# Kernel optimization log

Measured on AMD Instinct MI355X. Metric: run time of the kernel, lower is better.

The kernel has to match this reference:

```python
import jax, jax.numpy as jnp
import numpy as np

EPS = 1e-08

def rms_norm(x, eps=EPS):
    # Matches torch: mean-centered, population variance (unbiased=False)
    mean = jnp.mean(x, axis=-1, keepdims=True)
    var = jnp.var(x, axis=-1, keepdims=True)
    return (x - mean) / jnp.sqrt(var + eps)

def activation_quant(x):
    s = 127.0 / jnp.max(jnp.abs(x), axis=-1, keepdims=True)
    return jnp.clip(jnp.round(s * x), -128, 127) / s

def ternary_matmul(x, w):
    # pos_mask - neg_mask of sign(w) equals sign(w); x @ sign(w).T
    return jnp.matmul(x, jnp.sign(w).T)

def setup_inputs() -> dict:
    key = jax.random.key(0)
    k0, k1, k2, k3 = jax.random.split(key, 4)
    B, S, D, H = 4, 2048, 2048, 8192
    x = jax.random.normal(k0, (B, S, D), dtype=jnp.float32)
    W_g = jax.random.normal(k1, (H, D), dtype=jnp.float32) * 0.01
    W_u = jax.random.normal(k2, (H, D), dtype=jnp.float32) * 0.01
    W_d = jax.random.normal(k3, (D, H), dtype=jnp.float32) * 0.01
    return {"x": x, "W_g": W_g, "W_u": W_u, "W_d": W_d}

def reference(x, W_g, W_u, W_d):
    xq = activation_quant(rms_norm(x))
    g = jax.nn.silu(ternary_matmul(xq, W_g))   # [B,S,H]
    u = ternary_matmul(xq, W_u)                # [B,S,H]
    p = g * u
    return ternary_matmul(p, W_d)              # [B,S,D]
```

## Files before the change

### kernel.cpp

```cpp
#include <hip/hip_runtime.h>
#include <stdint.h>

#define MROWS 8192
#define DDIM  2048
#define HDIM  8192

typedef __attribute__((ext_vector_type(8))) short bf16x8;
typedef __attribute__((ext_vector_type(4))) float f32x4;
typedef __attribute__((ext_vector_type(4))) int   i32x4;
typedef unsigned short u16;

__device__ __forceinline__ void async_load16(const void* g, void* l) {
  auto gp = reinterpret_cast<const __attribute__((address_space(1))) unsigned int*>(
      reinterpret_cast<uintptr_t>(g));
  auto lp = reinterpret_cast<__attribute__((address_space(3))) unsigned int*>(
      reinterpret_cast<uintptr_t>(l));
  __builtin_amdgcn_global_load_lds(gp, lp, 16, 0, 0);
}

__device__ __forceinline__ u16 f2bf(float f) {
  union { float f; unsigned int u; } v; v.f = f;
  unsigned int r = v.u + 0x7FFF + ((v.u >> 16) & 1);
  return (u16)(r >> 16);
}

__global__ void sign_i8x2_kernel(const float* __restrict__ wg, const float* __restrict__ wu,
                                 char* __restrict__ og, char* __restrict__ ou) {
  const int t = blockIdx.x * 256 + threadIdx.x;
  const float* w = blockIdx.y ? wu : wg;
  char* o = blockIdx.y ? ou : og;
  const float4* w4 = (const float4*)w;
  float4 a = w4[t * 2], b = w4[t * 2 + 1];
  float v[8] = {a.x, a.y, a.z, a.w, b.x, b.y, b.z, b.w};
  union { char s[8]; uint2 u; } pk;
#pragma unroll
  for (int i = 0; i < 8; i++)
    pk.s[i] = v[i] > 0.f ? (char)1 : (v[i] < 0.f ? (char)-1 : (char)0);
  ((uint2*)o)[t] = pk.u;
}

__global__ void sign_bf16_kernel(const float* __restrict__ w, u16* __restrict__ o) {
  const int t = blockIdx.x * 256 + threadIdx.x;
  const float4* w4 = (const float4*)w;
  float4 a = w4[t * 2], b = w4[t * 2 + 1];
  float v[8] = {a.x, a.y, a.z, a.w, b.x, b.y, b.z, b.w};
  union { u16 s[8]; uint4 u; } pk;
#pragma unroll
  for (int i = 0; i < 8; i++)
    pk.s[i] = v[i] > 0.f ? 0x3F80 : (v[i] < 0.f ? 0xBF80 : 0);
  ((uint4*)o)[t] = pk.u;
}

__global__ void norm_quant_i8_kernel(const float* __restrict__ x,
                                     char* __restrict__ q, float* __restrict__ inv) {
  const int row  = blockIdx.x;
  const int tid  = threadIdx.x;
  const int lane = tid & 63, wave = tid >> 6;
  const float4* xr = (const float4*)(x + (size_t)row * DDIM);
  float4 a = xr[tid * 2], b = xr[tid * 2 + 1];
  float v[8] = {a.x, a.y, a.z, a.w, b.x, b.y, b.z, b.w};
  float s1 = 0.f, s2 = 0.f;
#pragma unroll
  for (int i = 0; i < 8; i++) { s1 += v[i]; s2 += v[i] * v[i]; }
#pragma unroll
  for (int o = 1; o < 64; o <<= 1) { s1 += __shfl_xor(s1, o); s2 += __shfl_xor(s2, o); }
  __shared__ float ssum[4], ssq[4], smax[4];
  if (lane == 0) { ssum[wave] = s1; ssq[wave] = s2; }
  __syncthreads();
  s1 = ssum[0] + ssum[1] + ssum[2] + ssum[3];
  s2 = ssq[0] + ssq[1] + ssq[2] + ssq[3];
  const float mean = s1 * (1.f / DDIM);
  const float var  = s2 * (1.f / DDIM) - mean * mean;
  const float rstd = rsqrtf(var + 1e-8f);
  float mx = 0.f;
#pragma unroll
  for (int i = 0; i < 8; i++) { v[i] = (v[i] - mean) * rstd; mx = fmaxf(mx, fabsf(v[i])); }
#pragma unroll
  for (int o = 1; o < 64; o <<= 1) mx = fmaxf(mx, __shfl_xor(mx, o));
  if (lane == 0) smax[wave] = mx;
  __syncthreads();
  mx = fmaxf(fmaxf(smax[0], smax[1]), fmaxf(smax[2], smax[3]));
  const float s = 127.f / mx;
  if (tid == 0) inv[row] = mx * (1.f / 127.f);
  union { char s8[8]; uint2 u; } pk;
#pragma unroll
  for (int i = 0; i < 8; i++) {
    float qq = rintf(v[i] * s);
    qq = fminf(fmaxf(qq, -128.f), 127.f);
    pk.s8[i] = (char)(int)qq;
  }
  ((uint2*)(q + (size_t)row * DDIM))[tid] = pk.u;
}

__global__ __launch_bounds__(512, 2) void gemm_glu_i8_kernel(
    const char* __restrict__ A,
    const char* __restrict__ Bg,
    const char* __restrict__ Bu,
    const float* __restrict__ inv,
    u16* __restrict__ P)
{
  constexpr int K  = DDIM;
  constexpr int NT = K / 128;
  const int l   = blockIdx.x + gridDim.x * blockIdx.y;
  const int xcd = l & 7;
  const int s_  = l >> 3;
  const int n0 = (xcd * 8 + (s_ & 7)) * 128;
  const int m0 = (s_ >> 3) * 256;
  const int tid  = threadIdx.x;
  const int lane = tid & 63, wave = tid >> 6;
  const int wm = wave >> 1, wn = wave & 1;
  const int quad = lane >> 4, l16 = lane & 15;

  __shared__ __align__(16) char lds[131072];

  i32x4 accg[4][4], accu[4][4];
  const i32x4 zero = {0, 0, 0, 0};
#pragma unroll
  for (int i = 0; i < 4; i++)
#pragma unroll
    for (int j = 0; j < 4; j++) { accg[i][j] = zero; accu[i][j] = zero; }

  const int arow = wm * 64 + l16;
  const int brow = wn * 64 + l16;
  const int swz  = (l16 & 7) << 4;

  const int rr  = tid >> 3;
  const int cbs = ((tid & 7) << 4) ^ ((rr & 7) << 4);
  const char* aSrc = A  + (size_t)(m0 + rr) * K + cbs;
  const char* gSrc = Bg + (size_t)(n0 + rr) * K + cbs;
  const char* uSrc = Bu + (size_t)(n0 + rr) * K + cbs;

#define STG_A(is) async_load16(aSrc + (size_t)(is) * 64 * K + k0n, bufN + (is) * 8192 + wave * 1024)
#define STG_G(is) async_load16(gSrc + (size_t)(is) * 64 * K + k0n, bufN + 32768 + (is) * 8192 + wave * 1024)
#define STG_U(is) async_load16(uSrc + (size_t)(is) * 64 * K + k0n, bufN + 49152 + (is) * 8192 + wave * 1024)
#define STG_TILE() do { STG_A(0); STG_A(1); STG_A(2); STG_A(3); \
                        STG_G(0); STG_G(1); STG_U(0); STG_U(1); } while (0)

  {
    char* bufN = lds;           const int k0n = 0;
    STG_TILE();
  }
  {
    char* bufN = lds + 65536;   const int k0n = 128;
    STG_TILE();
  }
  asm volatile("s_waitcnt vmcnt(8)" ::: "memory");
  __builtin_amdgcn_s_barrier();

  for (int t = 0; t < NT; ++t) {
    const char* bufC = lds + (size_t)(t & 1) * 65536;
    i32x4 a[4];
#pragma unroll
    for (int ks = 0; ks < 2; ++ks) {
#pragma unroll
      for (int jh = 0; jh < 2; ++jh) {
        const int koff = (ks * 64 + quad * 16) ^ swz;
        if (jh == 0) {
#pragma unroll
          for (int i = 0; i < 4; ++i)
            a[i] = *(const i32x4*)(bufC + (size_t)(arow + i * 16) * 128 + koff);
        }
        i32x4 bg[2], bu[2];
#pragma unroll
        for (int jj = 0; jj < 2; ++jj) {
          const int j = jh * 2 + jj;
          bg[jj] = *(const i32x4*)(bufC + 32768 + (size_t)(brow + j * 16) * 128 + koff);
          bu[jj] = *(const i32x4*)(bufC + 49152 + (size_t)(brow + j * 16) * 128 + koff);
        }
        __builtin_amdgcn_s_barrier();
        __builtin_amdgcn_s_setprio(1);
#pragma unroll
        for (int i = 0; i < 4; ++i)
#pragma unroll
          for (int jj = 0; jj < 2; ++jj) {
            const int j = jh * 2 + jj;
            accg[i][j] = __builtin_amdgcn_mfma_i32_16x16x64_i8(a[i], bg[jj], accg[i][j], 0, 0, 0);
            accu[i][j] = __builtin_amdgcn_mfma_i32_16x16x64_i8(a[i], bu[jj], accu[i][j], 0, 0, 0);
          }
        __builtin_amdgcn_s_setprio(0);
      }
    }
    __builtin_amdgcn_s_barrier();
    if (t + 2 < NT) {
      char* bufN = lds + (size_t)(t & 1) * 65536;
      const int k0n = (t + 2) * 128;
      STG_TILE();
      asm volatile("s_waitcnt vmcnt(8)" ::: "memory");
    } else {
      asm volatile("s_waitcnt vmcnt(0)" ::: "memory");
    }
    __builtin_amdgcn_s_barrier();
  }
#undef STG_A
#undef STG_G
#undef STG_U
#undef STG_TILE

  const int rbase = m0 + wm * 64 + quad * 4;
  const int cbase = n0 + wn * 64 + l16;
#pragma unroll
  for (int i = 0; i < 4; i++) {
    float iv[4];
#pragma unroll
    for (int r = 0; r < 4; r++) iv[r] = inv[rbase + i * 16 + r];
#pragma unroll
    for (int j = 0; j < 4; j++)
#pragma unroll
      for (int r = 0; r < 4; r++) {
        float g = (float)accg[i][j][r] * iv[r];
        float u = (float)accu[i][j][r] * iv[r];
        float pv = (g / (1.f + __expf(-g))) * u;
        P[(size_t)(rbase + i * 16 + r) * HDIM + (cbase + j * 16)] = f2bf(pv);
      }
  }
}

__global__ __launch_bounds__(512, 2) void gemm_out_kernel(
    const u16* __restrict__ A,
    const u16* __restrict__ B,
    float* __restrict__ C)
{
  constexpr size_t KB = (size_t)HDIM * 2;
  constexpr int NT = (int)(KB / 128);
  const int l   = blockIdx.x + gridDim.x * blockIdx.y;
  const int xcd = l & 7;
  const int s_  = l >> 3;
  const int n0 = xcd * 256;
  const int m0 = s_ * 256;
  const int tid  = threadIdx.x;
  const int lane = tid & 63, wave = tid >> 6;
  const int wm = wave >> 2, wn = wave & 3;
  const int quad = lane >> 4, l16 = lane & 15;

  __shared__ __align__(16) char lds[131072];

  f32x4 acc[8][4];
  const f32x4 zero = {0.f, 0.f, 0.f, 0.f};
#pragma unroll
  for (int i = 0; i < 8; i++)
#pragma unroll
    for (int j = 0; j < 4; j++) acc[i][j] = zero;

  const int arow = wm * 128 + l16;
  const int brow = wn * 64 + l16;
  const int swz  = (l16 & 7) << 4;

  const int rr  = tid >> 3;
  const int cbs = ((tid & 7) << 4) ^ ((rr & 7) << 4);
  const char* aSrc = (const char*)A + (size_t)(m0 + rr) * KB + cbs;
  const char* bSrc = (const char*)B + (size_t)(n0 + rr) * KB + cbs;

#define STG2_A(is) async_load16(aSrc + (size_t)(is) * 64 * KB + k0n, bufN + (is) * 8192 + wave * 1024)
#define STG2_B(is) async_load16(bSrc + (size_t)(is) * 64 * KB + k0n, bufN + 32768 + (is) * 8192 + wave * 1024)
#define STG2_TILE() do { STG2_A(0); STG2_A(1); STG2_A(2); STG2_A(3); \
                         STG2_B(0); STG2_B(1); STG2_B(2); STG2_B(3); } while (0)

  {
    char* bufN = lds;           const int k0n = 0;
    STG2_TILE();
  }
  {
    char* bufN = lds + 65536;   const int k0n = 128;
    STG2_TILE();
  }
  asm volatile("s_waitcnt vmcnt(8)" ::: "memory");
  __builtin_amdgcn_s_barrier();

  for (int t = 0; t < NT; ++t) {
    const char* bufC = lds + (size_t)(t & 1) * 65536;
    bf16x8 b[4];
#pragma unroll
    for (int ks = 0; ks < 2; ++ks) {
#pragma unroll
      for (int ih = 0; ih < 2; ++ih) {
        const int koff = (ks * 64 + quad * 16) ^ swz;
        if (ih == 0) {
#pragma unroll
          for (int j = 0; j < 4; ++j)
            b[j] = *(const bf16x8*)(bufC + 32768 + (size_t)(brow + j * 16) * 128 + koff);
        }
        bf16x8 a[4];
#pragma unroll
        for (int ii = 0; ii < 4; ++ii)
          a[ii] = *(const bf16x8*)(bufC + (size_t)(arow + (ih * 4 + ii) * 16) * 128 + koff);
        __builtin_amdgcn_s_barrier();
        __builtin_amdgcn_s_setprio(1);
#pragma unroll
        for (int ii = 0; ii < 4; ++ii) {
          const int i = ih * 4 + ii;
#pragma unroll
          for (int j = 0; j < 4; ++j)
            acc[i][j] = __builtin_amdgcn_mfma_f32_16x16x32_bf16(a[ii], b[j], acc[i][j], 0, 0, 0);
        }
        __builtin_amdgcn_s_setprio(0);
      }
    }
    __builtin_amdgcn_s_barrier();
    if (t + 2 < NT) {
      char* bufN = lds + (size_t)(t & 1) * 65536;
      const int k0n = (t + 2) * 128;
      STG2_TILE();
      asm volatile("s_waitcnt vmcnt(8)" ::: "memory");
    } else {
      asm volatile("s_waitcnt vmcnt(0)" ::: "memory");
    }
    __builtin_amdgcn_s_barrier();
  }
#undef STG2_A
#undef STG2_B
#undef STG2_TILE

  const int rbase = m0 + wm * 128 + quad * 4;
  const int cbase = n0 + wn * 64 + l16;
#pragma unroll
  for (int i = 0; i < 8; i++)
#pragma unroll
    for (int j = 0; j < 4; j++)
#pragma unroll
      for (int r = 0; r < 4; r++)
        C[(size_t)(rbase + i * 16 + r) * DDIM + (cbase + j * 16)] = acc[i][j][r];
}

extern "C" void kernel_launch(void* const* d_in, const int* in_sizes, int n_in,
                              void* d_out, int out_size, void* d_ws, size_t ws_size,
                              hipStream_t stream) {
  const float* x  = (const float*)d_in[0];
  const float* Wg = (const float*)d_in[1];
  const float* Wu = (const float*)d_in[2];
  const float* Wd = (const float*)d_in[3];

  char* ws = (char*)d_ws;
  char*  q    = ws;
  float* inv  = (float*)(ws + 16777216ull);
  char*  sWg  = ws + 20971520ull;
  char*  sWu  = ws + 37748736ull;
  u16*   sWd  = (u16*)(ws + 54525952ull);
  u16*   p    = (u16*)(ws + 88080384ull);
  float* out  = (float*)d_out;

  dim3 gs(8192, 2);
  sign_i8x2_kernel<<<gs, 256, 0, stream>>>(Wg, Wu, sWg, sWu);
  sign_bf16_kernel<<<8192, 256, 0, stream>>>(Wd, sWd);

  norm_quant_i8_kernel<<<MROWS, 256, 0, stream>>>(x, q, inv);

  dim3 g1(HDIM / 128, MROWS / 256);
  gemm_glu_i8_kernel<<<g1, 512, 0, stream>>>(q, sWg, sWu, inv, p);

  dim3 g2(DDIM / 256, MROWS / 256);
  gemm_out_kernel<<<g2, 512, 0, stream>>>(p, sWd, out);
}
```

Measured before the change: 759.9 us.

## Simplify GLU int8 GEMM to single-buffered 128x128 tiles with 256 threads

Replaces the double-buffered, two-tile-ahead prefetch pipeline in the gate/up int8 GEMM with a simple single-buffered loop. Each K step loads A, Bg and Bu into LDS and synchronizes before computing. The block tile shrinks from 256x128 to 128x128 with 4 waves, and LDS drops to 48KB, allowing more resident blocks per CU. In exchange, global load latency is no longer overlapped with MFMA work inside a block and must be hidden by occupancy instead.

```diff
diff --git a/kernel.cpp b/kernel.cpp
--- a/kernel.cpp
+++ b/kernel.cpp
@@ -92,26 +92,28 @@
   ((uint2*)(q + (size_t)row * DDIM))[tid] = pk.u;
 }
 
-__global__ __launch_bounds__(512, 2) void gemm_glu_i8_kernel(
+__global__ __launch_bounds__(256, 2) void gemm_glu_i8_kernel(
     const char* __restrict__ A,
     const char* __restrict__ Bg,
     const char* __restrict__ Bu,
     const float* __restrict__ inv,
     u16* __restrict__ P)
 {
-  constexpr int K  = DDIM;
-  constexpr int NT = K / 128;
+  constexpr int K = DDIM;
   const int l   = blockIdx.x + gridDim.x * blockIdx.y;
   const int xcd = l & 7;
   const int s_  = l >> 3;
   const int n0 = (xcd * 8 + (s_ & 7)) * 128;
-  const int m0 = (s_ >> 3) * 256;
+  const int m0 = (s_ >> 3) * 128;
   const int tid  = threadIdx.x;
   const int lane = tid & 63, wave = tid >> 6;
   const int wm = wave >> 1, wn = wave & 1;
   const int quad = lane >> 4, l16 = lane & 15;
 
-  __shared__ __align__(16) char lds[131072];
+  __shared__ __align__(16) char lds[49152];
+  char* lA  = lds;
+  char* lBg = lds + 16384;
+  char* lBu = lds + 32768;
 
   i32x4 accg[4][4], accu[4][4];
   const i32x4 zero = {0, 0, 0, 0};
@@ -122,79 +124,42 @@
 
   const int arow = wm * 64 + l16;
   const int brow = wn * 64 + l16;
-  const int swz  = (l16 & 7) << 4;
-
-  const int rr  = tid >> 3;
-  const int cbs = ((tid & 7) << 4) ^ ((rr & 7) << 4);
-  const char* aSrc = A  + (size_t)(m0 + rr) * K + cbs;
-  const char* gSrc = Bg + (size_t)(n0 + rr) * K + cbs;
-  const char* uSrc = Bu + (size_t)(n0 + rr) * K + cbs;
-
-#define STG_A(is) async_load16(aSrc + (size_t)(is) * 64 * K + k0n, bufN + (is) * 8192 + wave * 1024)
-#define STG_G(is) async_load16(gSrc + (size_t)(is) * 64 * K + k0n, bufN + 32768 + (is) * 8192 + wave * 1024)
-#define STG_U(is) async_load16(uSrc + (size_t)(is) * 64 * K + k0n, bufN + 49152 + (is) * 8192 + wave * 1024)
-#define STG_TILE() do { STG_A(0); STG_A(1); STG_A(2); STG_A(3); \
-                        STG_G(0); STG_G(1); STG_U(0); STG_U(1); } while (0)
-
-  {
-    char* bufN = lds;           const int k0n = 0;
-    STG_TILE();
-  }
-  {
-    char* bufN = lds + 65536;   const int k0n = 128;
-    STG_TILE();
-  }
-  asm volatile("s_waitcnt vmcnt(8)" ::: "memory");
-  __builtin_amdgcn_s_barrier();
-
-  for (int t = 0; t < NT; ++t) {
-    const char* bufC = lds + (size_t)(t & 1) * 65536;
-    i32x4 a[4];
+  const int aswz = (arow & 7) << 4;
+  const int bswz = (brow & 7) << 4;
+
+  for (int k0 = 0; k0 < K; k0 += 128) {
+    __syncthreads();
+#pragma unroll
+    for (int is = 0; is < 4; ++is) {
+      const int o   = is * 4096 + tid * 16;
+      const int r   = o >> 7;
+      const int cbs = (o & 127) ^ ((r & 7) << 4);
+      async_load16(A  + (size_t)(m0 + r) * K + k0 + cbs, lA  + is * 4096 + wave * 1024);
+      async_load16(Bg + (size_t)(n0 + r) * K + k0 + cbs, lBg + is * 4096 + wave * 1024);
+      async_load16(Bu + (size_t)(n0 + r) * K + k0 + cbs, lBu + is * 4096 + wave * 1024);
+    }
+    __syncthreads();
 #pragma unroll
     for (int ks = 0; ks < 2; ++ks) {
-#pragma unroll
-      for (int jh = 0; jh < 2; ++jh) {
-        const int koff = (ks * 64 + quad * 16) ^ swz;
-        if (jh == 0) {
-#pragma unroll
-          for (int i = 0; i < 4; ++i)
-            a[i] = *(const i32x4*)(bufC + (size_t)(arow + i * 16) * 128 + koff);
+      const int koff = ks * 64 + quad * 16;
+      i32x4 a[4], bg[4], bu[4];
+#pragma unroll
+      for (int i = 0; i < 4; i++)
+        a[i] = *(const i32x4*)(lA + (arow + i * 16) * 128 + (koff ^ aswz));
+#pragma unroll
+      for (int j = 0; j < 4; j++) {
+        bg[j] = *(const i32x4*)(lBg + (brow + j * 16) * 128 + (koff ^ bswz));
+        bu[j] = *(const i32x4*)(lBu + (brow + j * 16) * 128 + (koff ^ bswz));
+      }
+#pragma unroll
+      for (int i = 0; i < 4; i++)
+#pragma unroll
+        for (int j = 0; j < 4; j++) {
+          accg[i][j] = __builtin_amdgcn_mfma_i32_16x16x64_i8(a[i], bg[j], accg[i][j], 0, 0, 0);
+          accu[i][j] = __builtin_amdgcn_mfma_i32_16x16x64_i8(a[i], bu[j], accu[i][j], 0, 0, 0);
         }
-        i32x4 bg[2], bu[2];
-#pragma unroll
-        for (int jj = 0; jj < 2; ++jj) {
-          const int j = jh * 2 + jj;
-          bg[jj] = *(const i32x4*)(bufC + 32768 + (size_t)(brow + j * 16) * 128 + koff);
-          bu[jj] = *(const i32x4*)(bufC + 49152 + (size_t)(brow + j * 16) * 128 + koff);
-        }
-        __builtin_amdgcn_s_barrier();
-        __builtin_amdgcn_s_setprio(1);
-#pragma unroll
-        for (int i = 0; i < 4; ++i)
-#pragma unroll
-          for (int jj = 0; jj < 2; ++jj) {
-            const int j = jh * 2 + jj;
-            accg[i][j] = __builtin_amdgcn_mfma_i32_16x16x64_i8(a[i], bg[jj], accg[i][j], 0, 0, 0);
-            accu[i][j] = __builtin_amdgcn_mfma_i32_16x16x64_i8(a[i], bu[jj], accu[i][j], 0, 0, 0);
-          }
-        __builtin_amdgcn_s_setprio(0);
-      }
     }
-    __builtin_amdgcn_s_barrier();
-    if (t + 2 < NT) {
-      char* bufN = lds + (size_t)(t & 1) * 65536;
-      const int k0n = (t + 2) * 128;
-      STG_TILE();
-      asm volatile("s_waitcnt vmcnt(8)" ::: "memory");
-    } else {
-      asm volatile("s_waitcnt vmcnt(0)" ::: "memory");
-    }
-    __builtin_amdgcn_s_barrier();
-  }
-#undef STG_A
-#undef STG_G
-#undef STG_U
-#undef STG_TILE
+  }
 
   const int rbase = m0 + wm * 64 + quad * 4;
   const int cbase = n0 + wn * 64 + l16;
@@ -344,8 +309,8 @@
 
   norm_quant_i8_kernel<<<MROWS, 256, 0, stream>>>(x, q, inv);
 
-  dim3 g1(HDIM / 128, MROWS / 256);
-  gemm_glu_i8_kernel<<<g1, 512, 0, stream>>>(q, sWg, sWu, inv, p);
+  dim3 g1(HDIM / 128, MROWS / 128);
+  gemm_glu_i8_kernel<<<g1, 256, 0, stream>>>(q, sWg, sWu, inv, p);
 
   dim3 g2(DDIM / 256, MROWS / 256);
   gemm_out_kernel<<<g2, 512, 0, stream>>>(p, sWd, out);
```

Result: faster. 713.4 us (-6.1%).
